# Performance work log

Measured on AMD Instinct MI355X. Metric: run time of the kernel, lower is better.

Reference implementation:

```python
import jax, jax.numpy as jnp
import numpy as np

EPS = 1e-9
# exp factors for iterations i = 4,3,2,1,0,-1,-2 ; i == -2 -> 0.0
EXP_FACTORS = np.array([-(4.0 ** i) if i != -2 else 0.0 for i in range(4, -3, -1)], dtype=np.float32)


def setup_inputs() -> dict:
    key = jax.random.key(0)
    k1, k2 = jax.random.split(key)
    B, N, D = 16, 2048, 256
    preds = jax.random.normal(k1, (B, N, D), dtype=jnp.float32)
    labels = jax.random.normal(k2, (B, N, D), dtype=jnp.float32)
    return {"preds": preds, "labels": labels}


def _pairwise_dist(p1, p2):
    # [B,N,1] + [B,1,N] - 2 * p1 @ p2^T -> [B,N,N]
    p1_norm = jnp.sum(p1 * p1, axis=-1)[..., :, None]
    p2_norm = jnp.sum(p2 * p2, axis=-1)[..., None, :]
    return p1_norm + p2_norm - 2.0 * jnp.einsum('bnd,bmd->bnm', p1, p2)


def _approx_match(pwdist):
    B, N, _ = pwdist.shape
    match0 = jnp.zeros_like(pwdist)
    currency0 = jnp.ones((B, N, 1), dtype=pwdist.dtype)
    cost0 = jnp.ones((B, 1, N), dtype=pwdist.dtype)

    def body(carry, exp_factor):
        match, cost, currency = carry
        bids = jnp.exp(exp_factor * pwdist) * cost              # [B,N,N]
        bids = bids * currency / (jnp.sum(bids, axis=2, keepdims=True) + EPS)
        bid_wt = jnp.minimum(cost / (jnp.sum(bids, axis=1, keepdims=True) + EPS), 1.0)
        bids = bids * bid_wt
        match = match + bids
        cost = jnp.maximum(cost - jnp.sum(bids, axis=1, keepdims=True), 0.0)
        currency = jnp.maximum(currency - jnp.sum(bids, axis=2, keepdims=True), 0.0)
        return (match, cost, currency), None

    (match, _, _), _ = jax.lax.scan(body, (match0, cost0, currency0), jnp.asarray(EXP_FACTORS))
    return match


def reference(preds, labels):
    pwdist = _pairwise_dist(preds, labels)
    match = _approx_match(pwdist)
    return jnp.sum(match * pwdist)
```

## Files before the change

### kernel.cpp

```cpp
#include <hip/hip_runtime.h>
#include <cstdint>

#define B_ 16
#define N_ 2048
#define D_ 256
#define EPS_ 1e-9f

#define AS1 __attribute__((address_space(1)))
#define AS3 __attribute__((address_space(3)))

typedef float f4 __attribute__((ext_vector_type(4)));

__device__ float blockReduceSum(float x, float* red){
  int tid = threadIdx.x;
  red[tid] = x; __syncthreads();
  #pragma unroll
  for (int off = 128; off > 0; off >>= 1){
    if (tid < off) red[tid] += red[tid + off];
    __syncthreads();
  }
  float r = red[0]; __syncthreads();
  return r;
}

__global__ __launch_bounds__(256) void prep_kernel(
    const float* __restrict__ preds, const float* __restrict__ labels,
    unsigned char* __restrict__ pa8, unsigned char* __restrict__ pb8,
    float* __restrict__ pn, float* __restrict__ ln,
    float* __restrict__ cost, float* __restrict__ currency,
    int* __restrict__ dmin, float* __restrict__ Ppart,
    float* __restrict__ npart, float* __restrict__ out){
  int s = blockIdx.y;
  int tid = threadIdx.x;
  if (s == 0){
    int i = blockIdx.x * 256 + tid;
    if (i < B_ * N_){ cost[i] = 1.f; currency[i] = 1.f; }
    if (i < B_) dmin[i] = 0x7f7fffff;
    if (i == 0) out[0] = 0.f;
  }
  const float* src = s ? labels : preds;
  unsigned char* dst = s ? pb8 : pa8;
  float* norms = s ? ln : pn;
  int w = tid >> 6, lane = tid & 63;
  size_t row0 = (size_t)blockIdx.x * 16 + (size_t)w * 4;
  float4 v[4];
  #pragma unroll
  for (int q = 0; q < 4; q++)
    v[q] = ((const float4*)(src + (row0 + q) * D_))[lane];
  __shared__ f4 part[4][64];
  __shared__ float nred[4];
  f4 s4;
  s4[0] = v[0].x + v[1].x + v[2].x + v[3].x;
  s4[1] = v[0].y + v[1].y + v[2].y + v[3].y;
  s4[2] = v[0].z + v[1].z + v[2].z + v[3].z;
  s4[3] = v[0].w + v[1].w + v[2].w + v[3].w;
  float nsum = 0.f;
  #pragma unroll
  for (int q = 0; q < 4; q++){
    float sum = v[q].x*v[q].x + v[q].y*v[q].y + v[q].z*v[q].z + v[q].w*v[q].w;
    #pragma unroll
    for (int off = 32; off >= 1; off >>= 1) sum += __shfl_xor(sum, off);
    if (lane == 0){ norms[row0 + q] = sum; nsum += sum; }
    int pk = 0;
    pk = __builtin_amdgcn_cvt_pk_fp8_f32(v[q].x, v[q].y, pk, false);
    pk = __builtin_amdgcn_cvt_pk_fp8_f32(v[q].z, v[q].w, pk, true);
    ((unsigned int*)(dst + (row0 + q) * D_))[lane] = (unsigned int)pk;
  }
  part[w][lane] = s4;
  if (lane == 0) nred[w] = nsum;
  __syncthreads();
  if (tid < 64){
    f4 t = part[0][tid];
    #pragma unroll
    for (int q = 1; q < 4; q++){
      t[0] += part[q][tid][0]; t[1] += part[q][tid][1];
      t[2] += part[q][tid][2]; t[3] += part[q][tid][3];
    }
    *(f4*)(Ppart + ((size_t)s * 2048 + blockIdx.x) * 256 + tid * 4) = t;
  }
  if (tid == 0)
    npart[s * 2048 + blockIdx.x] = nred[0] + nred[1] + nred[2] + nred[3];
}

__global__ __launch_bounds__(512, 2) void gemm_minmax(
    const unsigned char* __restrict__ pa, const unsigned char* __restrict__ pbm,
    const float* __restrict__ pn, const float* __restrict__ ln,
    int* __restrict__ dmin)
{
  int lid = blockIdx.x;
  int xcd = lid & 7;
  int l = lid >> 3;
  int b = 2 * xcd + (l >> 4);
  int p = l & 15;
  int tn = (p & 7) * 256;
  int tmb = (p >> 3) * 1024;
  const unsigned char* A  = pa  + (size_t)b * N_ * D_;
  const unsigned char* Bm = pbm + (size_t)b * N_ * D_;
  __shared__ __align__(16) unsigned char Bs[256 * 256];
  __shared__ __align__(16) unsigned char As[2][256 * 128];
  __shared__ float minred[8];
  int tid = threadIdx.x, lane = tid & 63, w = tid >> 6;
  int wm = (w >> 2) * 128, wn = (w & 3) * 64;
  int quad = lane >> 4, l15 = lane & 15;

  {
    int rB = lane >> 4;
    int c  = lane & 15;
    #pragma unroll
    for (int q = 0; q < 8; q++){
      int R = q * 32 + w * 4;
      int r = R + rB;
      int gc = c ^ (r & 7);
      __builtin_amdgcn_global_load_lds(
          (const AS1 unsigned int*)(const void*)&Bm[(size_t)(tn + r) * D_ + gc * 16],
          (AS3 unsigned int*)(void*)&Bs[R * 256 + lane * 16], 16, 0, 0);
    }
  }
  int lr = lane >> 3, ch = lane & 7;
  int gch = (ch ^ lr) * 16;
  #pragma unroll
  for (int pq = 0; pq < 4; pq++){
    int R = pq * 64 + w * 8;
    __builtin_amdgcn_global_load_lds(
        (const AS1 unsigned int*)(const void*)&A[(size_t)(tmb + R + lr) * D_ + gch],
        (AS3 unsigned int*)(void*)&As[0][R * 128], 16, 0, 0);
  }

  f4 acc[8][4];
  #pragma unroll
  for (int i = 0; i < 8; i++)
    #pragma unroll
    for (int j = 0; j < 4; j++) acc[i][j] = (f4)0.f;

  float mind = 3.4e38f;
  float lnr[4];
  #pragma unroll
  for (int jj = 0; jj < 4; jj++)
    lnr[jj] = ln[(size_t)b * N_ + tn + wn + jj * 16 + l15];

  int buf = 0;
  for (int step = 0; step < 8; step++){
    __syncthreads();
    if (step < 7){
      int t1 = (step + 1) >> 1, k1 = (step + 1) & 1;
      #pragma unroll
      for (int pq = 0; pq < 4; pq++){
        int R = pq * 64 + w * 8;
        __builtin_amdgcn_global_load_lds(
            (const AS1 unsigned int*)(const void*)&A[(size_t)(tmb + t1 * 256 + R + lr) * D_ + k1 * 128 + gch],
            (AS3 unsigned int*)(void*)&As[buf ^ 1][R * 128], 16, 0, 0);
      }
    }
    int ki = step & 1;
    #pragma unroll
    for (int s = 0; s < 4; s++){
      long af[8], bf[4];
      int base = s * 2 + (quad >> 1);
      int sub = (quad & 1) * 8;
      #pragma unroll
      for (int i = 0; i < 8; i++){
        int ra = wm + i * 16 + l15;
        af[i] = *(const long*)(&As[buf][ra * 128 + ((base ^ (ra & 7)) * 16) + sub]);
      }
      int gB = ki * 8 + base;
      #pragma unroll
      for (int jj = 0; jj < 4; jj++){
        int rb = wn + jj * 16 + l15;
        bf[jj] = *(const long*)(&Bs[rb * 256 + ((gB ^ (rb & 7)) * 16) + sub]);
      }
      #pragma unroll
      for (int i = 0; i < 8; i++)
        #pragma unroll
        for (int jj = 0; jj < 4; jj++)
          acc[i][jj] = __builtin_amdgcn_mfma_f32_16x16x32_fp8_fp8(af[i], bf[jj], acc[i][jj], 0, 0, 0);
    }
    if (ki == 1){
      int t = step >> 1;
      int tm = tmb + t * 256;
      float4 pnr[8];
      #pragma unroll
      for (int i = 0; i < 8; i++)
        pnr[i] = *(const float4*)&pn[(size_t)b * N_ + tm + wm + i * 16 + quad * 4];
      #pragma unroll
      for (int i = 0; i < 8; i++){
        float pv[4] = {pnr[i].x, pnr[i].y, pnr[i].z, pnr[i].w};
        #pragma unroll
        for (int jj = 0; jj < 4; jj++){
          #pragma unroll
          for (int reg = 0; reg < 4; reg++){
            float v = pv[reg] + lnr[jj] - 2.f * acc[i][jj][reg];
            mind = fminf(mind, v);
            acc[i][jj][reg] = 0.f;
          }
        }
      }
    }
    buf ^= 1;
  }

  #pragma unroll
  for (int off = 32; off >= 1; off >>= 1) mind = fminf(mind, __shfl_xor(mind, off));
  if (lane == 0) minred[w] = mind;
  __syncthreads();
  if (tid == 0){
    float m = minred[0];
    #pragma unroll
    for (int q = 1; q < 8; q++) m = fminf(m, minred[q]);
    atomicMin(&dmin[b], __float_as_int(fmaxf(m, 0.f)));
  }
}

__global__ __launch_bounds__(256) void tail(
    const float* __restrict__ preds, const float* __restrict__ labels,
    const float* __restrict__ pn, const float* __restrict__ ln,
    float* __restrict__ cost, float* __restrict__ currency,
    const int* __restrict__ dmin, const float* __restrict__ Ppart,
    const float* __restrict__ npart, float* __restrict__ out)
{
  const float EF[6] = {-256.f, -64.f, -16.f, -4.f, -1.f, -0.25f};
  int b = blockIdx.x, tid = threadIdx.x;
  float dm = __int_as_float(dmin[b]);
  __shared__ float red[256];

  if (-0.25f * (dm - 16.f) < -55.f){
    float Pc = 0.f, Lc = 0.f;
    for (int k = 0; k < 128; k++){
      Pc += Ppart[((size_t)b * 128 + k) * 256 + tid];
      Lc += Ppart[((size_t)(2048 + b * 128 + k)) * 256 + tid];
    }
    float np = (tid < 128) ? npart[b * 128 + tid] : 0.f;
    float nl = (tid < 128) ? npart[2048 + b * 128 + tid] : 0.f;
    float Spn = blockReduceSum(np, red);
    float Sln = blockReduceSum(nl, red);
    float dot = blockReduceSum(Pc * Lc, red);
    if (tid == 0) atomicAdd(out, Spn + Sln - dot * (1.f / 1024.f));
    return;
  }

  __shared__ float alpha_l[N_];
  __shared__ float prow[D_];
  const float* A  = preds  + (size_t)b * N_ * D_;
  const float* Bm = labels + (size_t)b * N_ * D_;
  const float* pnb = pn + (size_t)b * N_;
  const float* lnb = ln + (size_t)b * N_;
  float* costb = cost + (size_t)b * N_;
  float* curb  = currency + (size_t)b * N_;
  for (int it = 0; it < 6; it++){
    float ef = EF[it];
    if (ef * (dm - 16.f) < -55.f) continue;
    float cost_c[8], colsum_c[8], bw_c[8], costnew_c[8];
    #pragma unroll
    for (int j = 0; j < 8; j++){ cost_c[j] = costb[j*256+tid]; colsum_c[j] = 0.f; }
    for (int r = 0; r < N_; r++){
      prow[tid] = A[(size_t)r * D_ + tid];
      __syncthreads();
      float s_c[8], rs = 0.f;
      for (int j = 0; j < 8; j++){
        int m = j*256+tid; float dot = 0.f;
        for (int k = 0; k < D_; k++) dot += prow[k] * Bm[(size_t)m * D_ + k];
        float d = pnb[r] + lnb[m] - 2.f*dot;
        float s = __expf(ef * d) * cost_c[j];
        s_c[j] = s; rs += s;
      }
      float tot = blockReduceSum(rs, red);
      float a = curb[r] / (tot + EPS_);
      if (tid == 0) alpha_l[r] = a;
      #pragma unroll
      for (int j = 0; j < 8; j++) colsum_c[j] += s_c[j] * a;
      __syncthreads();
    }
    #pragma unroll
    for (int j = 0; j < 8; j++){
      float cs = colsum_c[j];
      float bw = fminf(cost_c[j] / (cs + EPS_), 1.f);
      bw_c[j] = bw; costnew_c[j] = fmaxf(cost_c[j] - bw*cs, 0.f);
    }
    float contrib = 0.f;
    for (int r = 0; r < N_; r++){
      prow[tid] = A[(size_t)r * D_ + tid];
      __syncthreads();
      float a = alpha_l[r], rbs = 0.f;
      for (int j = 0; j < 8; j++){
        int m = j*256+tid; float dot = 0.f;
        for (int k = 0; k < D_; k++) dot += prow[k] * Bm[(size_t)m * D_ + k];
        float d = pnb[r] + lnb[m] - 2.f*dot;
        float bid = __expf(ef * d) * cost_c[j] * a * bw_c[j];
        rbs += bid; contrib += bid * d;
      }
      float tot = blockReduceSum(rbs, red);
      if (tid == 0) curb[r] = fmaxf(curb[r] - tot, 0.f);
      __syncthreads();
    }
    #pragma unroll
    for (int j = 0; j < 8; j++) costb[j*256+tid] = costnew_c[j];
    float ctot = blockReduceSum(contrib, red);
    if (tid == 0) atomicAdd(out, ctot);
    __syncthreads();
  }
  float s = 0.f;
  #pragma unroll
  for (int j = 0; j < 8; j++) s += costb[j*256+tid];
  float Sc = blockReduceSum(s, red);
  float sa = 0.f, spn = 0.f;
  #pragma unroll
  for (int j = 0; j < 8; j++){
    int i = j*256+tid;
    float a = curb[i] / (Sc + EPS_);
    alpha_l[i] = a; sa += a; spn += a * pnb[i];
  }
  float Sa  = blockReduceSum(sa, red);
  float Spn = blockReduceSum(spn, red);
  float Pc = 0.f;
  for (int r = 0; r < N_; r++)
    Pc += alpha_l[r] * A[(size_t)r * D_ + tid];
  __syncthreads();
  float sv = 0.f, sln = 0.f;
  #pragma unroll
  for (int j = 0; j < 8; j++){
    int i = j*256+tid;
    float c = costb[i];
    float bw = fminf(c / (c * Sa + EPS_), 1.f);
    float vv = c * bw;
    alpha_l[i] = vv; sv += vv; sln += vv * lnb[i];
  }
  float Sv  = blockReduceSum(sv, red);
  float Sln = blockReduceSum(sln, red);
  float Lc = 0.f;
  for (int m = 0; m < N_; m++)
    Lc += alpha_l[m] * Bm[(size_t)m * D_ + tid];
  float dot = blockReduceSum(Pc * Lc, red);
  if (tid == 0) atomicAdd(out, Spn * Sv + Sa * Sln - 2.f * dot);
}

extern "C" void kernel_launch(void* const* d_in, const int* in_sizes, int n_in,
                              void* d_out, int out_size, void* d_ws, size_t ws_size,
                              hipStream_t stream)
{
  const float* preds  = (const float*)d_in[0];
  const float* labels = (const float*)d_in[1];
  float* out = (float*)d_out;
  char* ws = (char*)d_ws;
  const size_t BN = (size_t)B_ * N_;
  size_t off = 0;
  float* cost     = (float*)(ws + off); off += BN * 4;
  float* currency = (float*)(ws + off); off += BN * 4;
  float* pn       = (float*)(ws + off); off += BN * 4;
  float* ln       = (float*)(ws + off); off += BN * 4;
  int*   dmin     = (int*)(ws + off);   off += 256;
  float* npart    = (float*)(ws + off); off += (size_t)2 * 2048 * 4;
  float* Ppart    = (float*)(ws + off); off += (size_t)2 * 2048 * 256 * 4;
  unsigned char* pa8 = (unsigned char*)(ws + off); off += BN * D_;
  unsigned char* pb8 = (unsigned char*)(ws + off); off += BN * D_;

  prep_kernel<<<dim3((unsigned)(BN / 16), 2), 256, 0, stream>>>(
      preds, labels, pa8, pb8, pn, ln, cost, currency, dmin, Ppart, npart, out);
  gemm_minmax<<<dim3(256), 512, 0, stream>>>(pa8, pb8, pn, ln, dmin);
  tail<<<dim3(B_), 256, 0, stream>>>(preds, labels, pn, ln, cost, currency, dmin,
                                     Ppart, npart, out);
}
```

Before: 136.9 us.

## Load A fragments directly from global memory instead of LDS double buffering

The gemm_minmax kernel drops the double-buffered LDS staging of the A tile and has each lane read its FP8 A fragments straight from global memory into registers, while B stays resident in LDS. This removes the per-step barriers and the 64KB As buffer, which frees shared memory and may allow more blocks per CU. In exchange, every A fragment is fetched from global or L2 by each of the four column waves with 8-byte uncoalesced-ish loads, and there is no longer any explicit prefetch overlapping the loads with MFMA work.

```diff
diff --git a/kernel.cpp b/kernel.cpp
--- a/kernel.cpp
+++ b/kernel.cpp
@@ -97,7 +97,6 @@
   const unsigned char* A  = pa  + (size_t)b * N_ * D_;
   const unsigned char* Bm = pbm + (size_t)b * N_ * D_;
   __shared__ __align__(16) unsigned char Bs[256 * 256];
-  __shared__ __align__(16) unsigned char As[2][256 * 128];
   __shared__ float minred[8];
   int tid = threadIdx.x, lane = tid & 63, w = tid >> 6;
   int wm = (w >> 2) * 128, wn = (w & 3) * 64;
@@ -116,53 +115,34 @@
           (AS3 unsigned int*)(void*)&Bs[R * 256 + lane * 16], 16, 0, 0);
     }
   }
-  int lr = lane >> 3, ch = lane & 7;
-  int gch = (ch ^ lr) * 16;
-  #pragma unroll
-  for (int pq = 0; pq < 4; pq++){
-    int R = pq * 64 + w * 8;
-    __builtin_amdgcn_global_load_lds(
-        (const AS1 unsigned int*)(const void*)&A[(size_t)(tmb + R + lr) * D_ + gch],
-        (AS3 unsigned int*)(void*)&As[0][R * 128], 16, 0, 0);
-  }
-
-  f4 acc[8][4];
-  #pragma unroll
-  for (int i = 0; i < 8; i++)
-    #pragma unroll
-    for (int j = 0; j < 4; j++) acc[i][j] = (f4)0.f;
-
-  float mind = 3.4e38f;
+
   float lnr[4];
   #pragma unroll
   for (int jj = 0; jj < 4; jj++)
     lnr[jj] = ln[(size_t)b * N_ + tn + wn + jj * 16 + l15];
 
-  int buf = 0;
-  for (int step = 0; step < 8; step++){
-    __syncthreads();
-    if (step < 7){
-      int t1 = (step + 1) >> 1, k1 = (step + 1) & 1;
-      #pragma unroll
-      for (int pq = 0; pq < 4; pq++){
-        int R = pq * 64 + w * 8;
-        __builtin_amdgcn_global_load_lds(
-            (const AS1 unsigned int*)(const void*)&A[(size_t)(tmb + t1 * 256 + R + lr) * D_ + k1 * 128 + gch],
-            (AS3 unsigned int*)(void*)&As[buf ^ 1][R * 128], 16, 0, 0);
-      }
-    }
-    int ki = step & 1;
-    #pragma unroll
-    for (int s = 0; s < 4; s++){
+  __syncthreads();
+
+  float mind = 3.4e38f;
+
+  for (int t = 0; t < 4; t++){
+    int tm = tmb + t * 256;
+    f4 acc[8][4];
+    #pragma unroll
+    for (int i = 0; i < 8; i++)
+      #pragma unroll
+      for (int j = 0; j < 4; j++) acc[i][j] = (f4)0.f;
+
+    const unsigned char* Ap = A + (size_t)(tm + wm + l15) * D_ + quad * 8;
+
+    #pragma unroll
+    for (int kc = 0; kc < 8; kc++){
       long af[8], bf[4];
-      int base = s * 2 + (quad >> 1);
+      #pragma unroll
+      for (int i = 0; i < 8; i++)
+        af[i] = *(const long*)(Ap + (size_t)i * 16 * D_ + kc * 32);
+      int gB = kc * 2 + (quad >> 1);
       int sub = (quad & 1) * 8;
-      #pragma unroll
-      for (int i = 0; i < 8; i++){
-        int ra = wm + i * 16 + l15;
-        af[i] = *(const long*)(&As[buf][ra * 128 + ((base ^ (ra & 7)) * 16) + sub]);
-      }
-      int gB = ki * 8 + base;
       #pragma unroll
       for (int jj = 0; jj < 4; jj++){
         int rb = wn + jj * 16 + l15;
@@ -174,28 +154,23 @@
         for (int jj = 0; jj < 4; jj++)
           acc[i][jj] = __builtin_amdgcn_mfma_f32_16x16x32_fp8_fp8(af[i], bf[jj], acc[i][jj], 0, 0, 0);
     }
-    if (ki == 1){
-      int t = step >> 1;
-      int tm = tmb + t * 256;
-      float4 pnr[8];
-      #pragma unroll
-      for (int i = 0; i < 8; i++)
-        pnr[i] = *(const float4*)&pn[(size_t)b * N_ + tm + wm + i * 16 + quad * 4];
-      #pragma unroll
-      for (int i = 0; i < 8; i++){
-        float pv[4] = {pnr[i].x, pnr[i].y, pnr[i].z, pnr[i].w};
+
+    float4 pnr[8];
+    #pragma unroll
+    for (int i = 0; i < 8; i++)
+      pnr[i] = *(const float4*)&pn[(size_t)b * N_ + tm + wm + i * 16 + quad * 4];
+    #pragma unroll
+    for (int i = 0; i < 8; i++){
+      float pv[4] = {pnr[i].x, pnr[i].y, pnr[i].z, pnr[i].w};
+      #pragma unroll
+      for (int jj = 0; jj < 4; jj++){
         #pragma unroll
-        for (int jj = 0; jj < 4; jj++){
-          #pragma unroll
-          for (int reg = 0; reg < 4; reg++){
-            float v = pv[reg] + lnr[jj] - 2.f * acc[i][jj][reg];
-            mind = fminf(mind, v);
-            acc[i][jj][reg] = 0.f;
-          }
+        for (int reg = 0; reg < 4; reg++){
+          float v = pv[reg] + lnr[jj] - 2.f * acc[i][jj][reg];
+          mind = fminf(mind, v);
         }
       }
     }
-    buf ^= 1;
   }
 
   #pragma unroll
```

Result: slower. 177.4 us (+29.6%).
